# Kernel tuning notes

Hardware: AMD Instinct MI355X
Metric: run time of the kernel (lower is better)

## Reference

```python
import jax, jax.numpy as jnp
import numpy as np

B, S, D = 1, 2048, 2048        # batch, max_seq_len, hidden_dim_attention
G, HPG = 4, 8                   # n_head_groups, n_heads_per_group
H = G * HPG                     # 32 total heads
DK = D // G                     # 512, KV projection width
HD = D // H                     # 64, head dim
EPS = 1e-6


def _embed_position(x, pm):
    # x: [B, S, d]; pm: [2, 1, S, D] -> uses pm[i][:, :, :d]
    d = x.shape[-1]
    _x = jnp.concatenate([-x[:, :, d // 2:], x[:, :, :d // 2]], axis=-1)
    # Faithful to source: BOTH terms use the rotated _x (source quirk).
    return _x * pm[0][:, :, :d] + _x * pm[1][:, :, :d]


def setup_inputs() -> dict:
    key = jax.random.key(0)
    k0, k1, k2, k3, k4, k5 = jax.random.split(key, 6)
    sc = 1.0 / np.sqrt(D).astype(np.float32)
    x = jax.random.normal(k0, (B, S, D), jnp.float32)
    position_matrix = jax.random.uniform(k1, (2, 1, S, D), jnp.float32)
    Wq = jax.random.normal(k2, (D, D), jnp.float32) * sc
    Wk = jax.random.normal(k3, (DK, D), jnp.float32) * sc
    Wv = jax.random.normal(k4, (DK, D), jnp.float32) * sc
    Wo = jax.random.normal(k5, (D, D), jnp.float32) * sc
    return {"x": x, "position_matrix": position_matrix,
            "Wq": Wq, "Wk": Wk, "Wv": Wv, "Wo": Wo}


def reference(x, position_matrix, Wq, Wk, Wv, Wo):
    xq = x @ Wq.T                                  # [B,S,D]
    xk = x @ Wk.T                                  # [B,S,DK]
    xv = x @ Wv.T                                  # [B,S,DK]
    xq = _embed_position(xq, position_matrix)
    xk = _embed_position(xk, position_matrix)
    # GQA expansion: replicate the DK-wide KV across G groups, split into heads.
    xk4 = jnp.broadcast_to(xk[:, :, None, :], (B, S, G, DK)).reshape(B, S, H, HD).transpose(0, 2, 1, 3)
    xv4 = jnp.broadcast_to(xv[:, :, None, :], (B, S, G, DK)).reshape(B, S, H, HD).transpose(0, 2, 1, 3)
    xq4 = xq.reshape(B, S, H, HD).transpose(0, 2, 1, 3)   # [B,H,S,HD]
    score = jnp.einsum('bhsd,bhtd->bhst', xq4, xk4) / (np.sqrt(DK) + EPS)
    # Source adds a tiny positive value (1e-10) above the diagonal, not -inf.
    mask = jnp.triu(jnp.full((S, S), 1e-10, jnp.float32), 1)
    score = score + mask
    e = jnp.exp(score.astype(jnp.float32))
    scores = (e / (jnp.sum(e, axis=-1, keepdims=True) + 1.0)).astype(xq4.dtype)
    out = jnp.einsum('bhst,bhtd->bhsd', scores, xv4)      # [B,H,S,HD]
    out = out.transpose(0, 2, 1, 3).reshape(B, S, D)
    return out @ Wo.T
```

## Files before the change

### kernel.cpp

```cpp
#include <hip/hip_runtime.h>
#include <cmath>

typedef unsigned short u16;
typedef unsigned int u32;
typedef __bf16 bf16x8 __attribute__((ext_vector_type(8)));
typedef __bf16 bf16x4 __attribute__((ext_vector_type(4)));
typedef float f32x4 __attribute__((ext_vector_type(4)));

#define S_LEN 2048
#define D_MODEL 2048
#define DK_ 512
#define PM1_OFF 4194304
#define CEXP 0.06375872f

__device__ __forceinline__ u16 f2b(float f) {
  u32 u = __float_as_uint(f);
  return (u16)((u + 0x7fffu + ((u >> 16) & 1u)) >> 16);
}

__device__ __forceinline__ void gload_lds16(const void* gp, void* lp) {
  __builtin_amdgcn_global_load_lds(
      (const __attribute__((address_space(1))) void*)gp,
      (__attribute__((address_space(3))) void*)lp, 16, 0, 0);
}

__device__ __forceinline__ void vmcnt0_barrier() {
  asm volatile("s_waitcnt vmcnt(0)" ::: "memory");
  __builtin_amdgcn_s_barrier();
}

__global__ __launch_bounds__(256) void cast_all_kernel(
    const float* __restrict__ x, const float* __restrict__ wq,
    const float* __restrict__ wk, const float* __restrict__ wv,
    const float* __restrict__ wo,
    u16* __restrict__ xb, u16* __restrict__ wqb, u16* __restrict__ wkb,
    u16* __restrict__ wvb, u16* __restrict__ wob)
{
  long i4 = (long)blockIdx.x * 256 + threadIdx.x;
  const float* src; u16* dst; long off;
  if (i4 < 1048576)       { src = x;  dst = xb;  off = i4; }
  else if (i4 < 2097152)  { src = wq; dst = wqb; off = i4 - 1048576; }
  else if (i4 < 2359296)  { src = wk; dst = wkb; off = i4 - 2097152; }
  else if (i4 < 2621440)  { src = wv; dst = wvb; off = i4 - 2359296; }
  else                    { src = wo; dst = wob; off = i4 - 2621440; }
  float4 v = *(const float4*)(src + off * 4);
  ushort4 o;
  o.x = f2b(v.x); o.y = f2b(v.y); o.z = f2b(v.z); o.w = f2b(v.w);
  *(ushort4*)(dst + off * 4) = o;
}

template<int EPI>
__global__ __launch_bounds__(256) void gemm_bt(
    const u16* __restrict__ A, const u16* __restrict__ B,
    void* __restrict__ C0, void* __restrict__ C1, void* __restrict__ C2,
    int M, int N, int K, const float* __restrict__ pm)
{
  __shared__ u16 As[2][64 * 64];
  __shared__ u16 Bs[2][128 * 64];
  const int tid = threadIdx.x;
  const int lane = tid & 63, w = tid >> 6;
  const int wr = w >> 1, wc = w & 1;
  const int l15 = lane & 15, l4 = lane >> 4;
  const int m0 = blockIdx.y * 64, n0 = blockIdx.x * 128;

  const int srow = tid >> 3;
  const int scol = ((tid & 7) ^ (srow & 7)) << 3;
  const int swz = (l15 & 7) << 3;
  const int ldsoff = (tid >> 6) << 10;
  const u16* gA = A + (size_t)(m0 + srow) * K + scol;
  const u16* gB = B + (size_t)(n0 + srow) * K + scol;

  const f32x4 z4 = {0.f, 0.f, 0.f, 0.f};
  f32x4 acc[2][4];
#pragma unroll
  for (int i = 0; i < 2; ++i)
#pragma unroll
    for (int j = 0; j < 4; ++j) acc[i][j] = z4;

  {
    char* la = (char*)As[0] + ldsoff;
    char* lb = (char*)Bs[0] + ldsoff;
#pragma unroll
    for (int i = 0; i < 2; ++i) gload_lds16(gA + (size_t)(i * 32) * K, la + i * 4096);
#pragma unroll
    for (int i = 0; i < 4; ++i) gload_lds16(gB + (size_t)(i * 32) * K, lb + i * 4096);
  }
  vmcnt0_barrier();

  const int NT = K >> 6;
  int cur = 0;
  for (int t = 0; t < NT; ++t) {
    if (t + 1 < NT) {
      const int kt = (t + 1) << 6;
      char* la = (char*)As[cur ^ 1] + ldsoff;
      char* lb = (char*)Bs[cur ^ 1] + ldsoff;
#pragma unroll
      for (int i = 0; i < 2; ++i) gload_lds16(gA + (size_t)(i * 32) * K + kt, la + i * 4096);
#pragma unroll
      for (int i = 0; i < 4; ++i) gload_lds16(gB + (size_t)(i * 32) * K + kt, lb + i * 4096);
    }
    const u16* as = As[cur];
    const u16* bs = Bs[cur];
#pragma unroll
    for (int ks = 0; ks < 2; ++ks) {
      bf16x8 a[2], b[4];
#pragma unroll
      for (int mt = 0; mt < 2; ++mt)
        a[mt] = *(const bf16x8*)(&as[(wr * 32 + mt * 16 + l15) * 64 + ((ks * 32 + l4 * 8) ^ swz)]);
#pragma unroll
      for (int nt = 0; nt < 4; ++nt)
        b[nt] = *(const bf16x8*)(&bs[(wc * 64 + nt * 16 + l15) * 64 + ((ks * 32 + l4 * 8) ^ swz)]);
#pragma unroll
      for (int mt = 0; mt < 2; ++mt)
#pragma unroll
        for (int nt = 0; nt < 4; ++nt)
          acc[mt][nt] = __builtin_amdgcn_mfma_f32_16x16x32_bf16(a[mt], b[nt], acc[mt][nt], 0, 0, 0);
    }
    vmcnt0_barrier();
    cur ^= 1;
  }

#pragma unroll
  for (int mt = 0; mt < 2; ++mt)
#pragma unroll
    for (int nt = 0; nt < 4; ++nt)
#pragma unroll
      for (int j = 0; j < 4; ++j) {
        const int m = m0 + wr * 32 + mt * 16 + l4 * 4 + j;
        const int n = n0 + wc * 64 + nt * 16 + l15;
        const float v = acc[mt][nt][j];
        if (EPI == 2) {
          ((float*)C0)[(size_t)m * N + n] = v;
        } else {
          if (n < 2048) {
            const int jj = (n < 1024) ? (n + 1024) : (n - 1024);
            const float sv = (n < 1024) ? v : -v;
            const float p = pm[(size_t)m * D_MODEL + jj] +
                            pm[PM1_OFF + (size_t)m * D_MODEL + jj];
            ((u16*)C0)[(size_t)m * D_MODEL + jj] = f2b(sv * p * CEXP);
          } else if (n < 2560) {
            const int nn = n - 2048;
            const int jj = (nn < 256) ? (nn + 256) : (nn - 256);
            const float sv = (nn < 256) ? v : -v;
            const float p = pm[(size_t)m * D_MODEL + jj] +
                            pm[PM1_OFF + (size_t)m * D_MODEL + jj];
            ((u16*)C1)[(size_t)m * DK_ + jj] = f2b(sv * p);
          } else {
            ((u16*)C2)[(size_t)m * DK_ + (n - 2560)] = f2b(v);
          }
        }
      }
}

__global__ __launch_bounds__(256) void transpose_bf16(
    const u16* __restrict__ in, u16* __restrict__ out, int R, int C)
{
  __shared__ u16 t[32][33];
  const int c0 = blockIdx.x * 32, r0 = blockIdx.y * 32;
  const int x = threadIdx.x, y = threadIdx.y;
#pragma unroll
  for (int j = 0; j < 32; j += 8)
    t[y + j][x] = in[(size_t)(r0 + y + j) * C + c0 + x];
  __syncthreads();
#pragma unroll
  for (int j = 0; j < 32; j += 8)
    out[(size_t)(c0 + y + j) * R + r0 + x] = t[x][y + j];
}

__global__ __launch_bounds__(256) void attn_kernel(
    const u16* __restrict__ Q, const u16* __restrict__ Kx,
    const u16* __restrict__ Vt, u16* __restrict__ O)
{
  __shared__ u16 Ks[2][64 * 64];
  __shared__ u16 Vs[2][64 * 64];
  __shared__ u16 Es[4 * 16 * 64];

  const int tid = threadIdx.x;
  const int lane = tid & 63, w = tid >> 6;
  const int l15 = lane & 15, l4 = lane >> 4;
  const int h = blockIdx.y;
  const int q0 = blockIdx.x * 64 + w * 16;
  const int hk = (h & 7) * 64;

  bf16x8 bq[2];
#pragma unroll
  for (int ks = 0; ks < 2; ++ks)
    bq[ks] = *(const bf16x8*)(Q + (size_t)(q0 + l15) * D_MODEL + h * 64 + ks * 32 + l4 * 8);

  bf16x8 b1;
#pragma unroll
  for (int i = 0; i < 8; ++i) b1[i] = (__bf16)1.0f;

  const f32x4 z4 = {0.f, 0.f, 0.f, 0.f};
  f32x4 o[4], dsum = z4;
#pragma unroll
  for (int nt = 0; nt < 4; ++nt) o[nt] = z4;

  u16* Ew = Es + w * (16 * 64);
  const int swz = (l15 & 7) << 3;
  const int srow = tid >> 3;
  const int scol = ((tid & 7) ^ (srow & 7)) << 3;
  const int ldsoff = w << 10;
  const u16* gK = Kx + (size_t)srow * DK_ + hk + scol;
  const u16* gV = Vt + (size_t)(hk + srow) * S_LEN + scol;

  {
    char* lK = (char*)Ks[0] + ldsoff;
    char* lV = (char*)Vs[0] + ldsoff;
    gload_lds16(gK,                        lK);
    gload_lds16(gK + (size_t)32 * DK_,     lK + 4096);
    gload_lds16(gV,                        lV);
    gload_lds16(gV + (size_t)32 * S_LEN,   lV + 4096);
  }
  vmcnt0_barrier();

  int cur = 0;
  for (int t0 = 0; t0 < S_LEN; t0 += 64) {
    if (t0 + 64 < S_LEN) {
      char* lK = (char*)Ks[cur ^ 1] + ldsoff;
      char* lV = (char*)Vs[cur ^ 1] + ldsoff;
      gload_lds16(gK + (size_t)(t0 + 64) * DK_,       lK);
      gload_lds16(gK + (size_t)(t0 + 96) * DK_,       lK + 4096);
      gload_lds16(gV + t0 + 64,                       lV);
      gload_lds16(gV + t0 + 64 + (size_t)32 * S_LEN,  lV + 4096);
    }
    const u16* ks_ = Ks[cur];
    const u16* vs_ = Vs[cur];

    f32x4 sT[4];
#pragma unroll
    for (int tf = 0; tf < 4; ++tf) sT[tf] = z4;
#pragma unroll
    for (int ks = 0; ks < 2; ++ks) {
      bf16x8 ak[4];
#pragma unroll
      for (int tf = 0; tf < 4; ++tf)
        ak[tf] = *(const bf16x8*)(&ks_[(tf * 16 + l15) * 64 + ((ks * 32 + l4 * 8) ^ swz)]);
      __builtin_amdgcn_s_setprio(1);
#pragma unroll
      for (int tf = 0; tf < 4; ++tf)
        sT[tf] = __builtin_amdgcn_mfma_f32_16x16x32_bf16(ak[tf], bq[ks], sT[tf], 0, 0, 0);
      __builtin_amdgcn_s_setprio(0);
    }

#pragma unroll
    for (int tf = 0; tf < 4; ++tf) {
      const float e0 = __builtin_amdgcn_exp2f(sT[tf][0]);
      const float e1 = __builtin_amdgcn_exp2f(sT[tf][1]);
      const float e2 = __builtin_amdgcn_exp2f(sT[tf][2]);
      const float e3 = __builtin_amdgcn_exp2f(sT[tf][3]);
      bf16x4 pk = {(__bf16)e0, (__bf16)e1, (__bf16)e2, (__bf16)e3};
      *(bf16x4*)(&Ew[l15 * 64 + ((tf * 16 + l4 * 4) ^ swz)]) = pk;
    }

#pragma unroll
    for (int ks = 0; ks < 2; ++ks) {
      const bf16x8 ae = *(const bf16x8*)(&Ew[l15 * 64 + ((ks * 32 + l4 * 8) ^ swz)]);
      bf16x8 bv[4];
#pragma unroll
      for (int nt = 0; nt < 4; ++nt)
        bv[nt] = *(const bf16x8*)(&vs_[(nt * 16 + l15) * 64 + ((ks * 32 + l4 * 8) ^ swz)]);
      __builtin_amdgcn_s_setprio(1);
#pragma unroll
      for (int nt = 0; nt < 4; ++nt)
        o[nt] = __builtin_amdgcn_mfma_f32_16x16x32_bf16(ae, bv[nt], o[nt], 0, 0, 0);
      dsum = __builtin_amdgcn_mfma_f32_16x16x32_bf16(ae, b1, dsum, 0, 0, 0);
      __builtin_amdgcn_s_setprio(0);
    }

    vmcnt0_barrier();
    cur ^= 1;
  }

  float dn[4];
#pragma unroll
  for (int j = 0; j < 4; ++j) dn[j] = dsum[j] + 1.0f;
#pragma unroll
  for (int nt = 0; nt < 4; ++nt)
#pragma unroll
    for (int j = 0; j < 4; ++j) {
      O[(size_t)(q0 + l4 * 4 + j) * D_MODEL + h * 64 + nt * 16 + l15] =
          f2b(o[nt][j] / dn[j]);
    }
}

extern "C" void kernel_launch(void* const* d_in, const int* in_sizes, int n_in,
                              void* d_out, int out_size, void* d_ws, size_t ws_size,
                              hipStream_t stream) {
  const float* x  = (const float*)d_in[0];
  const float* pm = (const float*)d_in[1];
  const float* Wq = (const float*)d_in[2];
  const float* Wk = (const float*)d_in[3];
  const float* Wv = (const float*)d_in[4];
  const float* Wo = (const float*)d_in[5];
  float* outp = (float*)d_out;
  char* ws = (char*)d_ws;

  const size_t MB = 1024 * 1024;
  u16* xb   = (u16*)(ws + 0 * MB);
  u16* wqb  = (u16*)(ws + 8 * MB);
  u16* wkb  = (u16*)(ws + 16 * MB);
  u16* wvb  = (u16*)(ws + 18 * MB);
  u16* wob  = (u16*)(ws + 20 * MB);
  u16* qro  = (u16*)(ws + 28 * MB);
  u16* kro  = (u16*)(ws + 36 * MB);
  u16* xvb  = (u16*)(ws + 38 * MB);
  u16* xvt  = (u16*)(ws + 40 * MB);
  u16* attn = (u16*)(ws + 42 * MB);
  const u16* wqkv = wqb;

  cast_all_kernel<<<14336, 256, 0, stream>>>(x, Wq, Wk, Wv, Wo, xb, wqb, wkb, wvb, wob);
  gemm_bt<1><<<dim3(24, 32), 256, 0, stream>>>(xb, wqkv, (void*)qro, (void*)kro,
                                               (void*)xvb, 2048, 3072, 2048, pm);
  transpose_bf16<<<dim3(16, 64), dim3(32, 8), 0, stream>>>(xvb, xvt, 2048, 512);
  attn_kernel<<<dim3(32, 32), 256, 0, stream>>>(qro, kro, xvt, attn);
  gemm_bt<2><<<dim3(16, 32), 256, 0, stream>>>(attn, wob, (void*)outp, nullptr,
                                               nullptr, 2048, 2048, 2048, nullptr);
}
```

Measured before the change: 142.8 us.

## Triple-buffer GEMM loads, shrink N tile, fuse V transpose into epilogue

The GEMM now keeps three LDS stages and waits with a partial vmcnt, so global loads for step t+2 stay in flight while step t computes. The N tile drops from 128 to 64, which doubles the grid for more parallelism but halves per-block reuse. The V projection epilogue writes its output already transposed as packed 4-element stores, so the separate transpose kernel and its launch are removed. The cost is more blocks re-reading A and different LDS usage per block.

New measurement: 160.8 us. +12.6%, slower.

```diff
diff --git a/kernel.cpp b/kernel.cpp
--- a/kernel.cpp
+++ b/kernel.cpp
@@ -22,11 +22,6 @@
   __builtin_amdgcn_global_load_lds(
       (const __attribute__((address_space(1))) void*)gp,
       (__attribute__((address_space(3))) void*)lp, 16, 0, 0);
-}
-
-__device__ __forceinline__ void vmcnt0_barrier() {
-  asm volatile("s_waitcnt vmcnt(0)" ::: "memory");
-  __builtin_amdgcn_s_barrier();
 }
 
 __global__ __launch_bounds__(256) void cast_all_kernel(
@@ -55,13 +50,13 @@
     void* __restrict__ C0, void* __restrict__ C1, void* __restrict__ C2,
     int M, int N, int K, const float* __restrict__ pm)
 {
-  __shared__ u16 As[2][64 * 64];
-  __shared__ u16 Bs[2][128 * 64];
+  __shared__ u16 As[3][64 * 64];
+  __shared__ u16 Bs[3][64 * 64];
   const int tid = threadIdx.x;
   const int lane = tid & 63, w = tid >> 6;
   const int wr = w >> 1, wc = w & 1;
   const int l15 = lane & 15, l4 = lane >> 4;
-  const int m0 = blockIdx.y * 64, n0 = blockIdx.x * 128;
+  const int m0 = blockIdx.y * 64, n0 = blockIdx.x * 64;
 
   const int srow = tid >> 3;
   const int scol = ((tid & 7) ^ (srow & 7)) << 3;
@@ -71,100 +66,93 @@
   const u16* gB = B + (size_t)(n0 + srow) * K + scol;
 
   const f32x4 z4 = {0.f, 0.f, 0.f, 0.f};
-  f32x4 acc[2][4];
+  f32x4 acc[2][2];
 #pragma unroll
   for (int i = 0; i < 2; ++i)
 #pragma unroll
-    for (int j = 0; j < 4; ++j) acc[i][j] = z4;
-
-  {
-    char* la = (char*)As[0] + ldsoff;
-    char* lb = (char*)Bs[0] + ldsoff;
-#pragma unroll
-    for (int i = 0; i < 2; ++i) gload_lds16(gA + (size_t)(i * 32) * K, la + i * 4096);
-#pragma unroll
-    for (int i = 0; i < 4; ++i) gload_lds16(gB + (size_t)(i * 32) * K, lb + i * 4096);
-  }
-  vmcnt0_barrier();
+    for (int j = 0; j < 2; ++j) acc[i][j] = z4;
+
+#define STAGE_G(bufi, kt) {                                         \
+    char* la = (char*)As[bufi] + ldsoff;                            \
+    char* lb = (char*)Bs[bufi] + ldsoff;                            \
+    gload_lds16(gA + (kt), la);                                     \
+    gload_lds16(gA + (size_t)32 * K + (kt), la + 4096);             \
+    gload_lds16(gB + (kt), lb);                                     \
+    gload_lds16(gB + (size_t)32 * K + (kt), lb + 4096); }
+
+  STAGE_G(0, 0);
+  STAGE_G(1, 64);
 
   const int NT = K >> 6;
-  int cur = 0;
+  int bc = 0;
   for (int t = 0; t < NT; ++t) {
-    if (t + 1 < NT) {
-      const int kt = (t + 1) << 6;
-      char* la = (char*)As[cur ^ 1] + ldsoff;
-      char* lb = (char*)Bs[cur ^ 1] + ldsoff;
-#pragma unroll
-      for (int i = 0; i < 2; ++i) gload_lds16(gA + (size_t)(i * 32) * K + kt, la + i * 4096);
-#pragma unroll
-      for (int i = 0; i < 4; ++i) gload_lds16(gB + (size_t)(i * 32) * K + kt, lb + i * 4096);
-    }
-    const u16* as = As[cur];
-    const u16* bs = Bs[cur];
+    if (t + 1 < NT) asm volatile("s_waitcnt vmcnt(4)" ::: "memory");
+    else            asm volatile("s_waitcnt vmcnt(0)" ::: "memory");
+    __builtin_amdgcn_s_barrier();
+    if (t + 2 < NT) {
+      int bn = bc + 2; if (bn >= 3) bn -= 3;
+      STAGE_G(bn, (size_t)(t + 2) << 6);
+    }
+    const u16* as = As[bc];
+    const u16* bt_ = Bs[bc];
 #pragma unroll
     for (int ks = 0; ks < 2; ++ks) {
-      bf16x8 a[2], b[4];
+      bf16x8 a[2], b[2];
 #pragma unroll
       for (int mt = 0; mt < 2; ++mt)
         a[mt] = *(const bf16x8*)(&as[(wr * 32 + mt * 16 + l15) * 64 + ((ks * 32 + l4 * 8) ^ swz)]);
 #pragma unroll
-      for (int nt = 0; nt < 4; ++nt)
-        b[nt] = *(const bf16x8*)(&bs[(wc * 64 + nt * 16 + l15) * 64 + ((ks * 32 + l4 * 8) ^ swz)]);
+      for (int nt = 0; nt < 2; ++nt)
+        b[nt] = *(const bf16x8*)(&bt_[(wc * 32 + nt * 16 + l15) * 64 + ((ks * 32 + l4 * 8) ^ swz)]);
 #pragma unroll
       for (int mt = 0; mt < 2; ++mt)
 #pragma unroll
-        for (int nt = 0; nt < 4; ++nt)
+        for (int nt = 0; nt < 2; ++nt)
           acc[mt][nt] = __builtin_amdgcn_mfma_f32_16x16x32_bf16(a[mt], b[nt], acc[mt][nt], 0, 0, 0);
     }
-    vmcnt0_barrier();
-    cur ^= 1;
+    if (++bc == 3) bc = 0;
   }
+#undef STAGE_G
 
 #pragma unroll
   for (int mt = 0; mt < 2; ++mt)
 #pragma unroll
-    for (int nt = 0; nt < 4; ++nt)
-#pragma unroll
-      for (int j = 0; j < 4; ++j) {
-        const int m = m0 + wr * 32 + mt * 16 + l4 * 4 + j;
-        const int n = n0 + wc * 64 + nt * 16 + l15;
-        const float v = acc[mt][nt][j];
-        if (EPI == 2) {
-          ((float*)C0)[(size_t)m * N + n] = v;
-        } else {
-          if (n < 2048) {
-            const int jj = (n < 1024) ? (n + 1024) : (n - 1024);
-            const float sv = (n < 1024) ? v : -v;
-            const float p = pm[(size_t)m * D_MODEL + jj] +
-                            pm[PM1_OFF + (size_t)m * D_MODEL + jj];
-            ((u16*)C0)[(size_t)m * D_MODEL + jj] = f2b(sv * p * CEXP);
-          } else if (n < 2560) {
-            const int nn = n - 2048;
-            const int jj = (nn < 256) ? (nn + 256) : (nn - 256);
-            const float sv = (nn < 256) ? v : -v;
-            const float p = pm[(size_t)m * D_MODEL + jj] +
-                            pm[PM1_OFF + (size_t)m * D_MODEL + jj];
-            ((u16*)C1)[(size_t)m * DK_ + jj] = f2b(sv * p);
-          } else {
-            ((u16*)C2)[(size_t)m * DK_ + (n - 2560)] = f2b(v);
-          }
+    for (int nt = 0; nt < 2; ++nt) {
+      const int mb = m0 + wr * 32 + mt * 16 + l4 * 4;
+      const int n = n0 + wc * 32 + nt * 16 + l15;
+      if (EPI == 2) {
+#pragma unroll
+        for (int j = 0; j < 4; ++j)
+          ((float*)C0)[(size_t)(mb + j) * N + n] = acc[mt][nt][j];
+      } else if (n >= 2560) {
+        const int c = n - 2560;
+        ushort4 q;
+        q.x = f2b(acc[mt][nt][0]); q.y = f2b(acc[mt][nt][1]);
+        q.z = f2b(acc[mt][nt][2]); q.w = f2b(acc[mt][nt][3]);
+        *(ushort4*)((u16*)C2 + (size_t)c * S_LEN + mb) = q;
+      } else if (n < 2048) {
+        const int jj = (n < 1024) ? (n + 1024) : (n - 1024);
+#pragma unroll
+        for (int j = 0; j < 4; ++j) {
+          const int m = mb + j;
+          const float sv = (n < 1024) ? acc[mt][nt][j] : -acc[mt][nt][j];
+          const float p = pm[(size_t)m * D_MODEL + jj] +
+                          pm[PM1_OFF + (size_t)m * D_MODEL + jj];
+          ((u16*)C0)[(size_t)m * D_MODEL + jj] = f2b(sv * p * CEXP);
+        }
+      } else {
+        const int nn = n - 2048;
+        const int jj = (nn < 256) ? (nn + 256) : (nn - 256);
+#pragma unroll
+        for (int j = 0; j < 4; ++j) {
+          const int m = mb + j;
+          const float sv = (nn < 256) ? acc[mt][nt][j] : -acc[mt][nt][j];
+          const float p = pm[(size_t)m * D_MODEL + jj] +
+                          pm[PM1_OFF + (size_t)m * D_MODEL + jj];
+          ((u16*)C1)[(size_t)m * DK_ + jj] = f2b(sv * p);
         }
       }
-}
-
-__global__ __launch_bounds__(256) void transpose_bf16(
-    const u16* __restrict__ in, u16* __restrict__ out, int R, int C)
-{
-  __shared__ u16 t[32][33];
-  const int c0 = blockIdx.x * 32, r0 = blockIdx.y * 32;
-  const int x = threadIdx.x, y = threadIdx.y;
-#pragma unroll
-  for (int j = 0; j < 32; j += 8)
-    t[y + j][x] = in[(size_t)(r0 + y + j) * C + c0 + x];
-  __syncthreads();
-#pragma unroll
-  for (int j = 0; j < 32; j += 8)
-    out[(size_t)(c0 + y + j) * R + r0 + x] = t[x][y + j];
+    }
 }
 
 __global__ __launch_bounds__(256) void attn_kernel(
@@ -212,7 +200,8 @@
     gload_lds16(gV,                        lV);
     gload_lds16(gV + (size_t)32 * S_LEN,   lV + 4096);
   }
-  vmcnt0_barrier();
+  asm volatile("s_waitcnt vmcnt(0)" ::: "memory");
+  __builtin_amdgcn_s_barrier();
 
   int cur = 0;
   for (int t0 = 0; t0 < S_LEN; t0 += 64) {
@@ -268,7 +257,8 @@
       __builtin_amdgcn_s_setprio(0);
     }
 
-    vmcnt0_barrier();
+    asm volatile("s_waitcnt vmcnt(0)" ::: "memory");
+    __builtin_amdgcn_s_barrier();
     cur ^= 1;
   }
 
@@ -304,16 +294,14 @@
   u16* wob  = (u16*)(ws + 20 * MB);
   u16* qro  = (u16*)(ws + 28 * MB);
   u16* kro  = (u16*)(ws + 36 * MB);
-  u16* xvb  = (u16*)(ws + 38 * MB);
   u16* xvt  = (u16*)(ws + 40 * MB);
   u16* attn = (u16*)(ws + 42 * MB);
   const u16* wqkv = wqb;
 
   cast_all_kernel<<<14336, 256, 0, stream>>>(x, Wq, Wk, Wv, Wo, xb, wqb, wkb, wvb, wob);
-  gemm_bt<1><<<dim3(24, 32), 256, 0, stream>>>(xb, wqkv, (void*)qro, (void*)kro,
-                                               (void*)xvb, 2048, 3072, 2048, pm);
-  transpose_bf16<<<dim3(16, 64), dim3(32, 8), 0, stream>>>(xvb, xvt, 2048, 512);
+  gemm_bt<1><<<dim3(48, 32), 256, 0, stream>>>(xb, wqkv, (void*)qro, (void*)kro,
+                                               (void*)xvt, 2048, 3072, 2048, pm);
   attn_kernel<<<dim3(32, 32), 256, 0, stream>>>(qro, kro, xvt, attn);
-  gemm_bt<2><<<dim3(16, 32), 256, 0, stream>>>(attn, wob, (void*)outp, nullptr,
+  gemm_bt<2><<<dim3(32, 32), 256, 0, stream>>>(attn, wob, (void*)outp, nullptr,
                                                nullptr, 2048, 2048, 2048, nullptr);
 }
```

## Fuse V transpose into QKV GEMM epilogue and remap workgroups per XCD

Applied to the files above, without the earlier changes.

The QKV GEMM epilogue now writes the V projection directly in transposed layout with a 4-element vector store, so the separate transpose kernel and its extra global round trip are gone. Both GEMMs and the attention kernel remap their linear block index so that consecutive tiles sharing operands land on the same XCD, which should improve L2 reuse on the multi-die GPU. The remap hardcodes a 32-row tile count and a grid divisible by 8. The transposed V store is strided across rows, which may coalesce poorly.

Measured after the change: 140.7 us, median of 2. About the same (-1.5%).

```diff
diff --git a/kernel.cpp b/kernel.cpp
--- a/kernel.cpp
+++ b/kernel.cpp
@@ -61,7 +61,12 @@
   const int lane = tid & 63, w = tid >> 6;
   const int wr = w >> 1, wc = w & 1;
   const int l15 = lane & 15, l4 = lane >> 4;
-  const int m0 = blockIdx.y * 64, n0 = blockIdx.x * 128;
+
+  const int nwg = gridDim.x * gridDim.y;
+  const int orig = blockIdx.y * gridDim.x + blockIdx.x;
+  const int lin2 = (orig & 7) * (nwg >> 3) + (orig >> 3);
+  const int m0 = (lin2 & 31) * 64;
+  const int n0 = (lin2 >> 5) * 128;
 
   const int srow = tid >> 3;
   const int scol = ((tid & 7) ^ (srow & 7)) << 3;
@@ -123,48 +128,42 @@
 #pragma unroll
   for (int mt = 0; mt < 2; ++mt)
 #pragma unroll
-    for (int nt = 0; nt < 4; ++nt)
-#pragma unroll
-      for (int j = 0; j < 4; ++j) {
-        const int m = m0 + wr * 32 + mt * 16 + l4 * 4 + j;
-        const int n = n0 + wc * 64 + nt * 16 + l15;
-        const float v = acc[mt][nt][j];
-        if (EPI == 2) {
-          ((float*)C0)[(size_t)m * N + n] = v;
-        } else {
-          if (n < 2048) {
-            const int jj = (n < 1024) ? (n + 1024) : (n - 1024);
-            const float sv = (n < 1024) ? v : -v;
-            const float p = pm[(size_t)m * D_MODEL + jj] +
-                            pm[PM1_OFF + (size_t)m * D_MODEL + jj];
-            ((u16*)C0)[(size_t)m * D_MODEL + jj] = f2b(sv * p * CEXP);
-          } else if (n < 2560) {
-            const int nn = n - 2048;
-            const int jj = (nn < 256) ? (nn + 256) : (nn - 256);
-            const float sv = (nn < 256) ? v : -v;
-            const float p = pm[(size_t)m * D_MODEL + jj] +
-                            pm[PM1_OFF + (size_t)m * D_MODEL + jj];
-            ((u16*)C1)[(size_t)m * DK_ + jj] = f2b(sv * p);
-          } else {
-            ((u16*)C2)[(size_t)m * DK_ + (n - 2560)] = f2b(v);
-          }
+    for (int nt = 0; nt < 4; ++nt) {
+      const int mb = m0 + wr * 32 + mt * 16 + l4 * 4;
+      const int n = n0 + wc * 64 + nt * 16 + l15;
+      if (EPI == 2) {
+#pragma unroll
+        for (int j = 0; j < 4; ++j)
+          ((float*)C0)[(size_t)(mb + j) * N + n] = acc[mt][nt][j];
+      } else if (n >= 2560) {
+        const int c = n - 2560;
+        ushort4 q;
+        q.x = f2b(acc[mt][nt][0]); q.y = f2b(acc[mt][nt][1]);
+        q.z = f2b(acc[mt][nt][2]); q.w = f2b(acc[mt][nt][3]);
+        *(ushort4*)((u16*)C2 + (size_t)c * S_LEN + mb) = q;
+      } else if (n < 2048) {
+        const int jj = (n < 1024) ? (n + 1024) : (n - 1024);
+#pragma unroll
+        for (int j = 0; j < 4; ++j) {
+          const int m = mb + j;
+          const float sv = (n < 1024) ? acc[mt][nt][j] : -acc[mt][nt][j];
+          const float p = pm[(size_t)m * D_MODEL + jj] +
+                          pm[PM1_OFF + (size_t)m * D_MODEL + jj];
+          ((u16*)C0)[(size_t)m * D_MODEL + jj] = f2b(sv * p * CEXP);
+        }
+      } else {
+        const int nn = n - 2048;
+        const int jj = (nn < 256) ? (nn + 256) : (nn - 256);
+#pragma unroll
+        for (int j = 0; j < 4; ++j) {
+          const int m = mb + j;
+          const float sv = (nn < 256) ? acc[mt][nt][j] : -acc[mt][nt][j];
+          const float p = pm[(size_t)m * D_MODEL + jj] +
+                          pm[PM1_OFF + (size_t)m * D_MODEL + jj];
+          ((u16*)C1)[(size_t)m * DK_ + jj] = f2b(sv * p);
         }
       }
-}
-
-__global__ __launch_bounds__(256) void transpose_bf16(
-    const u16* __restrict__ in, u16* __restrict__ out, int R, int C)
-{
-  __shared__ u16 t[32][33];
-  const int c0 = blockIdx.x * 32, r0 = blockIdx.y * 32;
-  const int x = threadIdx.x, y = threadIdx.y;
-#pragma unroll
-  for (int j = 0; j < 32; j += 8)
-    t[y + j][x] = in[(size_t)(r0 + y + j) * C + c0 + x];
-  __syncthreads();
-#pragma unroll
-  for (int j = 0; j < 32; j += 8)
-    out[(size_t)(c0 + y + j) * R + r0 + x] = t[x][y + j];
+    }
 }
 
 __global__ __launch_bounds__(256) void attn_kernel(
@@ -178,8 +177,11 @@
   const int tid = threadIdx.x;
   const int lane = tid & 63, w = tid >> 6;
   const int l15 = lane & 15, l4 = lane >> 4;
-  const int h = blockIdx.y;
-  const int q0 = blockIdx.x * 64 + w * 16;
+
+  const int orig = blockIdx.y * 32 + blockIdx.x;
+  const int lin2 = (orig & 7) * 128 + (orig >> 3);
+  const int h = lin2 >> 5;
+  const int q0 = (lin2 & 31) * 64 + w * 16;
   const int hk = (h & 7) * 64;
 
   bf16x8 bq[2];
@@ -304,15 +306,13 @@
   u16* wob  = (u16*)(ws + 20 * MB);
   u16* qro  = (u16*)(ws + 28 * MB);
   u16* kro  = (u16*)(ws + 36 * MB);
-  u16* xvb  = (u16*)(ws + 38 * MB);
   u16* xvt  = (u16*)(ws + 40 * MB);
   u16* attn = (u16*)(ws + 42 * MB);
   const u16* wqkv = wqb;
 
   cast_all_kernel<<<14336, 256, 0, stream>>>(x, Wq, Wk, Wv, Wo, xb, wqb, wkb, wvb, wob);
   gemm_bt<1><<<dim3(24, 32), 256, 0, stream>>>(xb, wqkv, (void*)qro, (void*)kro,
-                                               (void*)xvb, 2048, 3072, 2048, pm);
-  transpose_bf16<<<dim3(16, 64), dim3(32, 8), 0, stream>>>(xvb, xvt, 2048, 512);
+                                               (void*)xvt, 2048, 3072, 2048, pm);
   attn_kernel<<<dim3(32, 32), 256, 0, stream>>>(qro, kro, xvt, attn);
   gemm_bt<2><<<dim3(16, 32), 256, 0, stream>>>(attn, wob, (void*)outp, nullptr,
                                                nullptr, 2048, 2048, 2048, nullptr);
```
